# Performance work log

Hardware: AMD Instinct MI355X
Metric: run time of the kernel (lower is better)

The kernel has to match this reference:

```python
import jax, jax.numpy as jnp
import numpy as np
import math

ROPE_BASE = 10000.0
ALIBI_SLOPE = 2.0 ** (-8.0)  # _get_alibi_slopes(1) == [2**(-8*1/1)]


def _rope_cos_sin(T, d):
    inv_freq = 1.0 / (ROPE_BASE ** (jnp.arange(0, d, 2, dtype=jnp.float32) / d))
    t = jnp.arange(T, dtype=jnp.float32)
    freqs = jnp.einsum('i,j->ij', t, inv_freq)          # [T, d/2]
    emb = jnp.concatenate([freqs, freqs], axis=-1)      # [T, d]
    return jnp.cos(emb), jnp.sin(emb)


def _rotate_half(x):
    x1, x2 = jnp.split(x, 2, axis=-1)
    return jnp.concatenate([-x2, x1], axis=-1)


def setup_inputs() -> dict:
    key = jax.random.key(0)
    kq, kk, kv = jax.random.split(key, 3)
    B, T, H = 8, 2048, 256
    return {
        'q': jax.random.normal(kq, (B, T, H), dtype=jnp.float32),
        'k': jax.random.normal(kk, (B, T, H), dtype=jnp.float32),
        'v': jax.random.normal(kv, (B, T, H), dtype=jnp.float32),
    }


def reference(q, k, v):
    B, T, H = q.shape  # num_heads == 1, so head_dim == H
    cos, sin = _rope_cos_sin(T, H)                      # [T, H]
    qe = q * cos + _rotate_half(q) * sin                # [B, T, H]
    ke = k * cos + _rotate_half(k) * sin                # [B, T, H]

    scale = 1.0 / math.sqrt(H)
    scores = jnp.einsum('btd,bsd->bts', qe, ke) * scale  # [B, T, T]

    pos = jnp.arange(T)
    rel = (pos[None, :] - pos[:, None]).astype(jnp.float32)  # [T, T]
    alibi = (ALIBI_SLOPE * rel)[None, None, :, :]            # [1, 1, T, T]

    # torch broadcast: [B,T,T] + [1,1,T,T] -> [1,B,T,T]
    scores = scores + alibi
    attn = jax.nn.softmax(scores, axis=-1)              # [1, B, T, T]
    out = jnp.matmul(attn, v)                           # [1, B, T, H]
    return out
```

## Files before the change

### kernel.cpp

```cpp
#include <hip/hip_runtime.h>

#define B_ 8
#define T_ 2048
#define H_ 256
#define PSTR 40
#define SCALE2 0.0901684403f
#define SLOPE2 0.00563552752f
#define ELEMS ((size_t)B_ * T_ * H_)

typedef __attribute__((ext_vector_type(8))) short bf16x8;
typedef __attribute__((ext_vector_type(4))) float f32x4;

#define MFMA16(a, b, c) __builtin_amdgcn_mfma_f32_16x16x32_bf16((a), (b), (c), 0, 0, 0)

__device__ __forceinline__ ushort f2bf(float f) {
  unsigned u = __float_as_uint(f);
  u += 0x7FFFu + ((u >> 16) & 1u);
  return (ushort)(u >> 16);
}

__device__ __forceinline__ void gl_lds16(const ushort* g, ushort* l) {
  __builtin_amdgcn_global_load_lds(
      (const __attribute__((address_space(1))) unsigned int*)g,
      (__attribute__((address_space(3))) unsigned int*)l, 16, 0, 0);
}

__global__ void prep_kernel(const float* __restrict__ k, const float* __restrict__ v,
                            ushort* __restrict__ kt, ushort* __restrict__ vt) {
  __shared__ ushort tile[64][72];
  const int bid = blockIdx.x;
  const int tid = threadIdx.x;
  if (bid < 1024) {
    int idx = bid * 256 + tid;
    int d8 = idx & 15;
    int bt = idx >> 4;
    int t = bt & (T_ - 1);
    int b = bt >> 11;
    size_t base = (size_t)bt * H_ + d8 * 8;
    float4 a0 = *(const float4*)(k + base);
    float4 a1 = *(const float4*)(k + base + 4);
    float4 c0 = *(const float4*)(k + base + 128);
    float4 c1 = *(const float4*)(k + base + 132);
    float av[8] = {a0.x, a0.y, a0.z, a0.w, a1.x, a1.y, a1.z, a1.w};
    float cv[8] = {c0.x, c0.y, c0.z, c0.w, c1.x, c1.y, c1.z, c1.w};
    bf16x8 lo, hi;
#pragma unroll
    for (int e = 0; e < 8; ++e) {
      int j = d8 * 8 + e;
      float rv = (float)t * exp2f((float)j * -0.103810252959f) * 0.15915494309f;
      float fr = rv - floorf(rv);
      float sn = __builtin_amdgcn_sinf(fr), cs = __builtin_amdgcn_cosf(fr);
      lo[e] = (short)f2bf(av[e] * cs - cv[e] * sn);
      hi[e] = (short)f2bf(cv[e] * cs + av[e] * sn);
    }
    size_t kdst = (((size_t)(b * 64 + (t >> 5)) * 32 + d8) * 32 + (t & 31)) * 8;
    *(bf16x8*)(kt + kdst) = lo;
    *(bf16x8*)(kt + kdst + 4096) = hi;
  } else {
    int bid2 = bid - 1024;
    int b = bid2 >> 7, rem = bid2 & 127;
    int h0 = (rem >> 5) * 64, t0 = (rem & 31) * 64;
    int c4 = tid & 15, r0 = tid >> 4;
#pragma unroll
    for (int p = 0; p < 4; ++p) {
      int row = r0 + p * 16;
      const float4 f = *(const float4*)(v + ((size_t)(b * T_ + t0 + row)) * H_ + h0 + c4 * 4);
      ushort4 u;
      u.x = f2bf(f.x); u.y = f2bf(f.y); u.z = f2bf(f.z); u.w = f2bf(f.w);
      *(ushort4*)&tile[row][(c4 * 4) ^ (8 * ((row >> 3) & 7))] = u;
    }
    __syncthreads();
#pragma unroll
    for (int p = 0; p < 2; ++p) {
      int c = tid + p * 256;
      int h = c >> 3, tc = (c & 7) * 8;
      int xo = 8 * (c & 7);
      ushort4 u0, u1;
      u0.x = tile[tc + 0][h ^ xo]; u0.y = tile[tc + 1][h ^ xo];
      u0.z = tile[tc + 2][h ^ xo]; u0.w = tile[tc + 3][h ^ xo];
      u1.x = tile[tc + 4][h ^ xo]; u1.y = tile[tc + 5][h ^ xo];
      u1.z = tile[tc + 6][h ^ xo]; u1.w = tile[tc + 7][h ^ xo];
      int tg = t0 + tc;
      size_t dst = (((size_t)(b * 64 + (tg >> 5)) * 4 + ((tg >> 3) & 3)) * 256 + (h0 + h)) * 8;
      *(ushort4*)(vt + dst) = u0;
      *(ushort4*)(vt + dst + 4) = u1;
    }
  }
}

__global__ __launch_bounds__(512, 1)
void attn_kernel(const float* __restrict__ q, const ushort* __restrict__ kt,
                 const ushort* __restrict__ vt, float* __restrict__ out) {
  __shared__ __align__(16) char smem[141568];
  ushort* Kbase = (ushort*)smem;
  ushort* Vbase = (ushort*)(smem + 65536);
  ushort* Pbase = (ushort*)(smem + 131072);
  float*  Lsh   = (float*)(smem + 141312);
  float*  Ofl   = (float*)smem;

  const int tid = threadIdx.x;
  const int w = tid >> 6, lane = tid & 63, quad = lane >> 4, l16 = lane & 15;
  const int g = w >> 2;
  const int wl = w & 3;
  const int gt = tid & 255;
  const int b = blockIdx.x;
  const int q0 = blockIdx.y * 64;
  const int kvb0 = g * (T_ / 2);

  ushort* Ksh = Kbase + g * 16384;
  ushort* Vsh = Vbase + g * 16384;
  ushort* Psh = Pbase + w * (16 * PSTR);

  bf16x8 aq[8];
  {
    const float* qb = q + ((size_t)(b * T_) + q0 + wl * 16) * H_;
    const int t = q0 + wl * 16 + l16;
    float qv[8][8];
#pragma unroll
    for (int ks = 0; ks < 8; ++ks) {
      float4 x0 = *(const float4*)(qb + (size_t)l16 * H_ + ks * 32 + quad * 8);
      float4 x1 = *(const float4*)(qb + (size_t)l16 * H_ + ks * 32 + quad * 8 + 4);
      qv[ks][0] = x0.x; qv[ks][1] = x0.y; qv[ks][2] = x0.z; qv[ks][3] = x0.w;
      qv[ks][4] = x1.x; qv[ks][5] = x1.y; qv[ks][6] = x1.z; qv[ks][7] = x1.w;
    }
#pragma unroll
    for (int ks = 0; ks < 4; ++ks)
#pragma unroll
      for (int e = 0; e < 8; ++e) {
        int d = ks * 32 + quad * 8 + e;
        float rv = (float)t * exp2f((float)d * -0.103810252959f) * 0.15915494309f;
        float fr = rv - floorf(rv);
        float sn = __builtin_amdgcn_sinf(fr), cs = __builtin_amdgcn_cosf(fr);
        aq[ks][e]     = (short)f2bf(qv[ks][e] * cs - qv[ks + 4][e] * sn);
        aq[ks + 4][e] = (short)f2bf(qv[ks + 4][e] * cs + qv[ks][e] * sn);
      }
  }

  const f32x4 fzero = {0.f, 0.f, 0.f, 0.f};
  f32x4 O[16], lac = fzero;
#pragma unroll
  for (int ht = 0; ht < 16; ++ht) O[ht] = fzero;
  bf16x8 vones;
#pragma unroll
  for (int i = 0; i < 8; ++i) vones[i] = (short)0x3F80;

  const ushort* ktb = kt + (size_t)(b * 64 + g * 32) * 8192;
  const ushort* vtb = vt + (size_t)(b * 64 + g * 32) * 8192;
  const int stoff = gt * 8;

#pragma unroll
  for (int tt = 0; tt < 2; ++tt) {
    const ushort* kg = ktb + (size_t)tt * 8192;
    const ushort* vg = vtb + (size_t)tt * 8192;
#pragma unroll
    for (int i = 0; i < 4; ++i) {
      gl_lds16(kg + stoff + i * 2048, Ksh + tt * 8192 + stoff + i * 2048);
      gl_lds16(vg + stoff + i * 2048, Vsh + tt * 8192 + stoff + i * 2048);
    }
  }

  const float arb = SLOPE2 * (float)(q0 + wl * 16 + quad * 4);

  for (int it = 0; it < 32; ++it) {
    const int p = it & 1;
    __builtin_amdgcn_sched_barrier(0);
    if (it == 31) __builtin_amdgcn_s_waitcnt(0x0070);
    else          __builtin_amdgcn_s_waitcnt(0x0F78);
    __builtin_amdgcn_s_barrier();
    __builtin_amdgcn_sched_barrier(0);

    f32x4 s[2] = {fzero, fzero};
#pragma unroll
    for (int ks = 0; ks < 8; ++ks)
#pragma unroll
      for (int nt = 0; nt < 2; ++nt) {
        bf16x8 kf = *(const bf16x8*)&Ksh[p * 8192 + ((ks * 4 + quad) * 32 + nt * 16 + l16) * 8];
        s[nt] = MFMA16(aq[ks], kf, s[nt]);
      }

#pragma unroll
    for (int nt = 0; nt < 2; ++nt) {
      float ac = SLOPE2 * (float)(kvb0 + it * 32 + nt * 16 + l16);
#pragma unroll
      for (int r = 0; r < 4; ++r) {
        float a0 = ac - arb - SLOPE2 * (float)r;
        float pv = __builtin_amdgcn_exp2f(fmaf(s[nt][r], SCALE2, a0));
        Psh[(quad * 4 + r) * PSTR + nt * 16 + l16] = f2bf(pv);
      }
    }

    bf16x8 pf = *(const bf16x8*)&Psh[l16 * PSTR + quad * 8];
    lac = MFMA16(pf, vones, lac);
#pragma unroll
    for (int ht = 0; ht < 16; ++ht) {
      bf16x8 vf = *(const bf16x8*)&Vsh[p * 8192 + (quad * 256 + ht * 16 + l16) * 8];
      O[ht] = MFMA16(pf, vf, O[ht]);
    }

    __builtin_amdgcn_sched_barrier(0);
    __builtin_amdgcn_s_waitcnt(0xC07F);
    __builtin_amdgcn_s_barrier();
    __builtin_amdgcn_sched_barrier(0);

    if (it < 30) {
      const ushort* kg = ktb + (size_t)(it + 2) * 8192;
      const ushort* vg = vtb + (size_t)(it + 2) * 8192;
#pragma unroll
      for (int i = 0; i < 4; ++i) {
        gl_lds16(kg + stoff + i * 2048, Ksh + p * 8192 + stoff + i * 2048);
        gl_lds16(vg + stoff + i * 2048, Vsh + p * 8192 + stoff + i * 2048);
      }
    }
  }

  if (g == 1) {
#pragma unroll
    for (int r = 0; r < 4; ++r) {
      int row = wl * 16 + quad * 4 + r;
#pragma unroll
      for (int ht = 0; ht < 16; ++ht)
        Ofl[row * 260 + ht * 16 + l16] = O[ht][r];
      if (l16 == 0) Lsh[row] = lac[r];
    }
  }
  __syncthreads();
  if (g == 0) {
    float* ob = out + ((size_t)(b * T_) + q0 + wl * 16) * H_;
#pragma unroll
    for (int r = 0; r < 4; ++r) {
      int row = wl * 16 + quad * 4 + r;
      float inv = 1.0f / (lac[r] + Lsh[row]);
#pragma unroll
      for (int ht = 0; ht < 16; ++ht)
        ob[(size_t)(quad * 4 + r) * H_ + ht * 16 + l16] =
            (O[ht][r] + Ofl[row * 260 + ht * 16 + l16]) * inv;
    }
  }
}

extern "C" void kernel_launch(void* const* d_in, const int* in_sizes, int n_in,
                              void* d_out, int out_size, void* d_ws, size_t ws_size,
                              hipStream_t stream) {
  const float* q = (const float*)d_in[0];
  const float* k = (const float*)d_in[1];
  const float* v = (const float*)d_in[2];
  float* out = (float*)d_out;

  ushort* kt = (ushort*)d_ws;
  ushort* vt = kt + ELEMS;

  prep_kernel<<<dim3(2048), 256, 0, stream>>>(k, v, kt, vt);
  attn_kernel<<<dim3(B_, T_ / 64), 512, 0, stream>>>(q, kt, vt, out);
}
```

Baseline: 144.6 us.

## Load V fragments directly to registers and triple-buffer K in LDS

V tiles are no longer staged through LDS. Each wave now loads its V MFMA fragments straight from global memory into registers, prefetching the next tile after the PV MMAs. K moves from double to triple buffering, which lets the second per-iteration barrier go, and LDS use shrinks. In exchange every wave fetches V redundantly from global or L2, register pressure rises from holding 16 extra bf16x8 values, and global-load latency now sits directly in front of the MFMAs.

```diff
diff --git a/kernel.cpp b/kernel.cpp
--- a/kernel.cpp
+++ b/kernel.cpp
@@ -91,11 +91,10 @@
 __global__ __launch_bounds__(512, 1)
 void attn_kernel(const float* __restrict__ q, const ushort* __restrict__ kt,
                  const ushort* __restrict__ vt, float* __restrict__ out) {
-  __shared__ __align__(16) char smem[141568];
+  __shared__ __align__(16) char smem[108800];
   ushort* Kbase = (ushort*)smem;
-  ushort* Vbase = (ushort*)(smem + 65536);
-  ushort* Pbase = (ushort*)(smem + 131072);
-  float*  Lsh   = (float*)(smem + 141312);
+  ushort* Pbase = (ushort*)(smem + 98304);
+  float*  Lsh   = (float*)(smem + 108544);
   float*  Ofl   = (float*)smem;
 
   const int tid = threadIdx.x;
@@ -107,8 +106,7 @@
   const int q0 = blockIdx.y * 64;
   const int kvb0 = g * (T_ / 2);
 
-  ushort* Ksh = Kbase + g * 16384;
-  ushort* Vsh = Vbase + g * 16384;
+  ushort* Kgrp = Kbase + g * 24576;
   ushort* Psh = Pbase + w * (16 * PSTR);
 
   bf16x8 aq[8];
@@ -147,34 +145,39 @@
   const ushort* ktb = kt + (size_t)(b * 64 + g * 32) * 8192;
   const ushort* vtb = vt + (size_t)(b * 64 + g * 32) * 8192;
   const int stoff = gt * 8;
-
-#pragma unroll
-  for (int tt = 0; tt < 2; ++tt) {
-    const ushort* kg = ktb + (size_t)tt * 8192;
-    const ushort* vg = vtb + (size_t)tt * 8192;
-#pragma unroll
-    for (int i = 0; i < 4; ++i) {
-      gl_lds16(kg + stoff + i * 2048, Ksh + tt * 8192 + stoff + i * 2048);
-      gl_lds16(vg + stoff + i * 2048, Vsh + tt * 8192 + stoff + i * 2048);
-    }
-  }
+  const int vro = (quad * 256 + l16) * 8;
+
+#pragma unroll
+  for (int i = 0; i < 4; ++i)
+    gl_lds16(ktb + stoff + i * 2048, Kgrp + stoff + i * 2048);
+  __builtin_amdgcn_sched_barrier(0);
+  bf16x8 vr[16];
+#pragma unroll
+  for (int ht = 0; ht < 16; ++ht)
+    vr[ht] = *(const bf16x8*)(vtb + vro + ht * 128);
+  __builtin_amdgcn_sched_barrier(0);
+#pragma unroll
+  for (int i = 0; i < 4; ++i)
+    gl_lds16(ktb + 8192 + stoff + i * 2048, Kgrp + 8192 + stoff + i * 2048);
 
   const float arb = SLOPE2 * (float)(q0 + wl * 16 + quad * 4);
 
   for (int it = 0; it < 32; ++it) {
-    const int p = it & 1;
-    __builtin_amdgcn_sched_barrier(0);
-    if (it == 31) __builtin_amdgcn_s_waitcnt(0x0070);
-    else          __builtin_amdgcn_s_waitcnt(0x0F78);
+    const int c = it % 3;
+    __builtin_amdgcn_sched_barrier(0);
+    if (it == 31) __builtin_amdgcn_s_waitcnt(0x0F70);
+    else          __builtin_amdgcn_s_waitcnt(0x0F74);
     __builtin_amdgcn_s_barrier();
     __builtin_amdgcn_sched_barrier(0);
 
+    const ushort* Kc = Kgrp + c * 8192;
+
     f32x4 s[2] = {fzero, fzero};
 #pragma unroll
     for (int ks = 0; ks < 8; ++ks)
 #pragma unroll
       for (int nt = 0; nt < 2; ++nt) {
-        bf16x8 kf = *(const bf16x8*)&Ksh[p * 8192 + ((ks * 4 + quad) * 32 + nt * 16 + l16) * 8];
+        bf16x8 kf = *(const bf16x8*)&Kc[((ks * 4 + quad) * 32 + nt * 16 + l16) * 8];
         s[nt] = MFMA16(aq[ks], kf, s[nt]);
       }
 
@@ -192,27 +195,27 @@
     bf16x8 pf = *(const bf16x8*)&Psh[l16 * PSTR + quad * 8];
     lac = MFMA16(pf, vones, lac);
 #pragma unroll
-    for (int ht = 0; ht < 16; ++ht) {
-      bf16x8 vf = *(const bf16x8*)&Vsh[p * 8192 + (quad * 256 + ht * 16 + l16) * 8];
-      O[ht] = MFMA16(pf, vf, O[ht]);
-    }
-
-    __builtin_amdgcn_sched_barrier(0);
-    __builtin_amdgcn_s_waitcnt(0xC07F);
-    __builtin_amdgcn_s_barrier();
-    __builtin_amdgcn_sched_barrier(0);
-
+    for (int ht = 0; ht < 16; ++ht)
+      O[ht] = MFMA16(pf, vr[ht], O[ht]);
+
+    __builtin_amdgcn_sched_barrier(0);
+    if (it < 31) {
+      const ushort* vg = vtb + (size_t)(it + 1) * 8192;
+#pragma unroll
+      for (int ht = 0; ht < 16; ++ht)
+        vr[ht] = *(const bf16x8*)(vg + vro + ht * 128);
+    }
+    __builtin_amdgcn_sched_barrier(0);
     if (it < 30) {
       const ushort* kg = ktb + (size_t)(it + 2) * 8192;
-      const ushort* vg = vtb + (size_t)(it + 2) * 8192;
-#pragma unroll
-      for (int i = 0; i < 4; ++i) {
-        gl_lds16(kg + stoff + i * 2048, Ksh + p * 8192 + stoff + i * 2048);
-        gl_lds16(vg + stoff + i * 2048, Vsh + p * 8192 + stoff + i * 2048);
-      }
-    }
-  }
-
+      ushort* kd = Kgrp + ((it + 2) % 3) * 8192;
+#pragma unroll
+      for (int i = 0; i < 4; ++i)
+        gl_lds16(kg + stoff + i * 2048, kd + stoff + i * 2048);
+    }
+  }
+
+  __syncthreads();
   if (g == 1) {
 #pragma unroll
     for (int r = 0; r < 4; ++r) {
```

Result: slower. 163.3 us (+12.9%).
